# Optimization experiments

Hardware: AMD Instinct MI355X
Metric: run time of the kernel (lower is better)

Reference implementation:

```python
import jax, jax.numpy as jnp
import numpy as np

B, T, D, P = 4, 2048, 1024, 128

def setup_inputs() -> dict:
    key = jax.random.key(0)
    ks = jax.random.split(key, 10)
    inp = {
        "x": jax.random.normal(ks[0], (B, T, D), dtype=jnp.float32),
        "Q_filt": jax.random.normal(ks[1], (P, P), dtype=jnp.float32),
        "K_filt": jax.random.normal(ks[2], (P, P), dtype=jnp.float32),
        "W_in": jax.random.normal(ks[3], (D, P), dtype=jnp.float32) / np.sqrt(D),
        "b_in": jax.random.normal(ks[4], (P,), dtype=jnp.float32) * 0.01,
        "W_v": jax.random.normal(ks[5], (D, P), dtype=jnp.float32) / np.sqrt(D),
        "b_v": jax.random.normal(ks[6], (P,), dtype=jnp.float32) * 0.01,
        "W_o": jax.random.normal(ks[7], (P, D), dtype=jnp.float32) / np.sqrt(P),
        "b_o": jax.random.normal(ks[8], (D,), dtype=jnp.float32) * 0.01,
        "decay": jnp.ones((T,), dtype=jnp.float32),
    }
    return inp

def reference(x, Q_filt, K_filt, W_in, b_in, W_v, b_v, W_o, b_o, decay):
    # x: (B,T,D)
    x_proj = x @ W_in + b_in          # (B,T,P)
    Q = x_proj @ Q_filt               # (B,T,P)
    K = x_proj @ K_filt               # (B,T,P)
    V = x @ W_v + b_v                 # (B,T,P)
    # outer-product state per timestep, scaled by per-step decay
    Z = jnp.einsum('bti,btj->btij', V, K) * decay[None, :, None, None]
    H = jnp.cumsum(Z, axis=1)         # (B,T,P,P) cumulative linear-attn state
    Y = jnp.einsum('bti,btij->btj', Q, H)  # (B,T,P)
    return Y @ W_o + b_o              # (B,T,D)
```

## Files before the change

kernel.cpp:

```cpp
#include <hip/hip_runtime.h>

#define BB 4
#define TT 2048
#define DD 1024
#define PP 128
#define NC 16
#define CH 128

typedef __attribute__((ext_vector_type(8))) short bf16x8;
typedef __attribute__((ext_vector_type(4))) float f32x4;

__device__ inline ushort f2bf(float f) {
  unsigned u = __builtin_bit_cast(unsigned, f);
  u = (u + 0x7FFF + ((u >> 16) & 1)) >> 16;
  return (ushort)u;
}
__device__ inline float bf2f(ushort u) {
  unsigned v = ((unsigned)u) << 16;
  return __builtin_bit_cast(float, v);
}

__device__ inline void gll16(const void* g, void* l) {
  __builtin_amdgcn_global_load_lds(
      (const __attribute__((address_space(1))) void*)g,
      (__attribute__((address_space(3))) void*)l, 16, 0, 0);
}

__device__ inline int swzoff(int row, int kbyte) {
  return row * 256 + (kbyte ^ ((row & 7) << 4));
}
__device__ inline int swz128(int row, int kbyte) {
  return row * 128 + (kbyte ^ ((row & 7) << 4));
}

template <int NI, int NT>
__device__ inline void stage_swz(const ushort* __restrict__ g, int ld, int koff,
                                 char* lds, int tid) {
#pragma unroll
  for (int j = 0; j < NI; ++j) {
    int L = j * (NT * 16) + tid * 16;
    int row = L >> 8;
    int off = (L & 255) ^ ((row & 7) << 4);
    gll16(g + (size_t)row * ld + koff + (off >> 1),
          lds + j * (NT * 16) + ((tid & (NT - 64)) << 4));
  }
}
template <int NI, int NT>
__device__ inline void stage_swz128(const ushort* __restrict__ g, int ld,
                                    int koff, char* lds, int tid) {
#pragma unroll
  for (int j = 0; j < NI; ++j) {
    int L = j * (NT * 16) + tid * 16;
    int row = L >> 7;
    int off = (L & 127) ^ ((row & 7) << 4);
    gll16(g + (size_t)row * ld + koff + (off >> 1),
          lds + j * (NT * 16) + ((tid & (NT - 64)) << 4));
  }
}

__device__ inline bf16x8 ld_swz(const char* lds, int row, int kbyte) {
  return *(const bf16x8*)(lds + swzoff(row, kbyte));
}
__device__ inline bf16x8 ld_swz128(const char* lds, int row, int kbyte) {
  return *(const bf16x8*)(lds + swz128(row, kbyte));
}

__device__ inline bf16x8 pack8(const float4& a, const float4& b) {
  bf16x8 v;
  v[0] = (short)f2bf(a.x); v[1] = (short)f2bf(a.y);
  v[2] = (short)f2bf(a.z); v[3] = (short)f2bf(a.w);
  v[4] = (short)f2bf(b.x); v[5] = (short)f2bf(b.y);
  v[6] = (short)f2bf(b.z); v[7] = (short)f2bf(b.w);
  return v;
}

__global__ __launch_bounds__(256) void prep_t(
    const float* __restrict__ Qf, const float* __restrict__ Kf,
    const float* __restrict__ W_in, const float* __restrict__ b_in,
    const float* __restrict__ W_v, const float* __restrict__ b_v,
    const float* __restrict__ W_o, ushort* __restrict__ WcatT,
    ushort* __restrict__ QKcT, ushort* __restrict__ WoT,
    float* __restrict__ bcat) {
  const int bid = blockIdx.x;
  const int t = threadIdx.x;
  if (bid == 104) {
    bcat[t] = (t < 128) ? b_in[t] : b_v[t - 128];
    return;
  }
  const float* src;
  ushort* dst;
  int ld_src, ld_dst, nn0;
  if (bid < 64) {
    int tn = bid >> 4, tk = bid & 15;
    src = (tn < 2) ? W_in : W_v;
    nn0 = (tn & 1) * 64;
    ld_src = 128;
    src += (size_t)(tk * 64) * 128;
    dst = WcatT + (size_t)(tn * 64) * 1024 + tk * 64;
    ld_dst = 1024;
  } else if (bid < 96) {
    int j = bid - 64, tn = j >> 1, tk = j & 1;
    src = W_o;
    nn0 = tn * 64;
    ld_src = 1024;
    src += (size_t)(tk * 64) * 1024;
    dst = WoT + (size_t)(tn * 64) * 128 + tk * 64;
    ld_dst = 128;
  } else {
    int j = bid - 96, tn = j >> 1, tk = j & 1;
    src = (tn < 2) ? Qf : Kf;
    nn0 = (tn & 1) * 64;
    ld_src = 128;
    src += (size_t)(tk * 64) * 128;
    dst = QKcT + (size_t)(tn * 64) * 128 + tk * 64;
    ld_dst = 128;
  }
  __shared__ ushort Tt[64][68];
  const int kr = t >> 4, nc = (t & 15) * 4;
#pragma unroll
  for (int p = 0; p < 4; ++p) {
    float4 v = *(const float4*)&src[(size_t)(p * 16 + kr) * ld_src + nn0 + nc];
    Tt[p * 16 + kr][nc + 0] = f2bf(v.x);
    Tt[p * 16 + kr][nc + 1] = f2bf(v.y);
    Tt[p * 16 + kr][nc + 2] = f2bf(v.z);
    Tt[p * 16 + kr][nc + 3] = f2bf(v.w);
  }
  __syncthreads();
  const int nr = t >> 4, kc = (t & 15) * 4;
#pragma unroll
  for (int p = 0; p < 4; ++p) {
    ushort4 o;
    o.x = Tt[kc + 0][p * 16 + nr];
    o.y = Tt[kc + 1][p * 16 + nr];
    o.z = Tt[kc + 2][p * 16 + nr];
    o.w = Tt[kc + 3][p * 16 + nr];
    *(ushort4*)&dst[(size_t)(p * 16 + nr) * ld_dst + kc] = o;
  }
}

__global__ __launch_bounds__(512) void gemm_xw(
    const float* __restrict__ x, const ushort* __restrict__ WcatT,
    const ushort* __restrict__ QKcT, const float* __restrict__ bcat,
    const float* __restrict__ decay, ushort* __restrict__ Qb,
    ushort* __restrict__ KdT, ushort* __restrict__ V,
    ushort* __restrict__ VT) {
  __shared__ char sm[81920];
  const int bid = blockIdx.x;
  const int swz = (bid & 7) * 32 + (bid >> 3);
  const int bm = (swz >> 1) * 64;
  const int bn = (swz & 1) * 128;
  const int tid = threadIdx.x, w = tid >> 6, l = tid & 63;
  const int wr = w >> 2, wc = w & 3, lr = l & 15, lk = l >> 4;

  const int arow = tid >> 3;
  const int acol = (tid & 7) * 8;
  const float* Ax = x + (size_t)(bm + arow) * DD + acol;
  const ushort* Bg = WcatT + (size_t)bn * DD;

  float4 ra[2];
  f32x4 z = {0.f, 0.f, 0.f, 0.f};
  f32x4 acc[2][2];
#pragma unroll
  for (int m = 0; m < 2; ++m)
#pragma unroll
    for (int n = 0; n < 2; ++n) acc[m][n] = z;

#define LOADA(t)                                                 \
  {                                                              \
    const float4* p = (const float4*)(Ax + (((t) & 15) << 6));   \
    ra[0] = p[0];                                                \
    ra[1] = p[1];                                                \
  }
#define WRITEA(lds) \
  { *(bf16x8*)((lds) + swz128(arow, acol * 2)) = pack8(ra[0], ra[1]); }

  LOADA(0);
  stage_swz128<2, 512>(Bg, DD, 0, sm + 8192, tid);
  asm volatile("s_waitcnt vmcnt(2)" ::: "memory");
  WRITEA(sm);
  LOADA(1);

  int cur = 0;
  for (int t = 0; t < 16; ++t) {
    char* nxt = sm + (cur ^ 1) * 24576;
    stage_swz128<2, 512>(Bg, DD, ((t + 1) & 15) << 6, nxt + 8192, tid);
    asm volatile("s_waitcnt vmcnt(2)" ::: "memory");
    WRITEA(nxt);
    LOADA(t + 2);
    asm volatile("s_waitcnt lgkmcnt(0)" ::: "memory");
    __builtin_amdgcn_s_barrier();
    const char* cp = sm + cur * 24576;
#pragma unroll
    for (int ks = 0; ks < 2; ++ks) {
      const int kb = ks * 64 + lk * 16;
      bf16x8 af[2], bfp[2];
#pragma unroll
      for (int m = 0; m < 2; ++m)
        af[m] = ld_swz128(cp, wr * 32 + m * 16 + lr, kb);
#pragma unroll
      for (int n = 0; n < 2; ++n)
        bfp[n] = ld_swz128(cp + 8192, wc * 32 + n * 16 + lr, kb);
#pragma unroll
      for (int m = 0; m < 2; ++m)
#pragma unroll
        for (int n = 0; n < 2; ++n)
          acc[m][n] = __builtin_amdgcn_mfma_f32_16x16x32_bf16(af[m], bfp[n], acc[m][n], 0, 0, 0);
    }
    __builtin_amdgcn_s_barrier();
    cur ^= 1;
  }
  asm volatile("s_waitcnt vmcnt(0)" ::: "memory");
  __syncthreads();
#undef LOADA
#undef WRITEA

  if (bn == 0) {
#pragma unroll
    for (int m = 0; m < 2; ++m)
#pragma unroll
      for (int n = 0; n < 2; ++n) {
        const int rowl = wr * 32 + m * 16 + lk * 4;
        const int col = wc * 32 + n * 16 + lr;
        const float bv = bcat[col];
#pragma unroll
        for (int j = 0; j < 4; ++j)
          *(ushort*)(sm + swzoff(rowl + j, col * 2)) = f2bf(acc[m][n][j] + bv);
      }
    stage_swz<8, 512>(QKcT, PP, 0, sm + 16384, tid);
    __syncthreads();

    f32x4 a2[2][4];
#pragma unroll
    for (int m = 0; m < 2; ++m)
#pragma unroll
      for (int n = 0; n < 4; ++n) a2[m][n] = z;
#pragma unroll
    for (int ks = 0; ks < 4; ++ks) {
      const int kb = ks * 64 + lk * 16;
      bf16x8 af[2], bfp[4];
#pragma unroll
      for (int m = 0; m < 2; ++m)
        af[m] = ld_swz(sm, wr * 32 + m * 16 + lr, kb);
#pragma unroll
      for (int n = 0; n < 4; ++n)
        bfp[n] = ld_swz(sm + 16384, wc * 64 + n * 16 + lr, kb);
#pragma unroll
      for (int m = 0; m < 2; ++m)
#pragma unroll
        for (int n = 0; n < 4; ++n)
          a2[m][n] = __builtin_amdgcn_mfma_f32_16x16x32_bf16(af[m], bfp[n], a2[m][n], 0, 0, 0);
    }
    __syncthreads();

#pragma unroll
    for (int m = 0; m < 2; ++m)
#pragma unroll
      for (int n = 0; n < 4; ++n) {
        const int rowl = wr * 32 + m * 16 + lk * 4;
        const int col = wc * 64 + n * 16 + lr;
        if (col < 128) {
#pragma unroll
          for (int j = 0; j < 4; ++j)
            Qb[(size_t)(bm + rowl + j) * PP + col] = f2bf(a2[m][n][j]);
        } else {
          const int cc = col - 128;
#pragma unroll
          for (int j = 0; j < 4; ++j) {
            float v = a2[m][n][j] * decay[(bm + rowl + j) & (TT - 1)];
            *(ushort*)(sm + 16384 + swz128(cc, (rowl + j) * 2)) = f2bf(v);
          }
        }
      }
    __syncthreads();

    {
      const int cc = tid >> 2;
#pragma unroll
      for (int i = 0; i < 2; ++i) {
        const int ch = (tid & 3) * 2 + i;
        bf16x8 v = ld_swz128(sm + 16384, cc, ch * 16);
        *(bf16x8*)&KdT[(size_t)cc * (BB * TT) + bm + ch * 8] = v;
      }
    }
  } else {
    ushort(*VTt)[72] = (ushort(*)[72]) & sm[0];
#pragma unroll
    for (int m = 0; m < 2; ++m)
#pragma unroll
      for (int n = 0; n < 2; ++n) {
        const int tl = wr * 32 + m * 16 + lk * 4;
        const int cc = wc * 32 + n * 16 + lr;
        const float bv = bcat[128 + cc];
#pragma unroll
        for (int j = 0; j < 4; ++j) {
          ushort u = f2bf(acc[m][n][j] + bv);
          V[(size_t)(bm + tl + j) * PP + cc] = u;
          VTt[cc][tl + j] = u;
        }
      }
    __syncthreads();
    const int row = tid >> 2;
#pragma unroll
    for (int i = 0; i < 2; ++i) {
      const int ch = (tid & 3) * 2 + i;
      bf16x8 v = *(const bf16x8*)&VTt[row][ch * 8];
      *(bf16x8*)&VT[(size_t)row * (BB * TT) + bm + ch * 8] = v;
    }
  }
}

__global__ __launch_bounds__(256) void chunk_state(
    const ushort* __restrict__ KdT, const ushort* __restrict__ VT,
    ushort* __restrict__ Scb) {
  const int p = blockIdx.x;
  const int xcd = p & 7, idx = p >> 3;
  const int bc = xcd + 8 * (idx >> 2);
  const int q = idx & 3;
  const int qj = q >> 1, qi = q & 1;
  const size_t r0 = (size_t)(bc >> 4) * TT + (bc & 15) * CH;
  const int tid = threadIdx.x, w = tid >> 6, l = tid & 63;
  const int wr = w >> 1, wc = w & 1, lr = l & 15, lk = l >> 4;

  f32x4 z = {0.f, 0.f, 0.f, 0.f};
  f32x4 acc[2][2];
#pragma unroll
  for (int m = 0; m < 2; ++m)
#pragma unroll
    for (int n = 0; n < 2; ++n) acc[m][n] = z;
#pragma unroll
  for (int ks = 0; ks < 4; ++ks) {
    const int kk = ks * 32 + lk * 8;
    bf16x8 af[2], bf[2];
#pragma unroll
    for (int m = 0; m < 2; ++m)
      af[m] = *(const bf16x8*)&KdT[(size_t)(qj * 64 + wr * 32 + m * 16 + lr) * (BB * TT) + r0 + kk];
#pragma unroll
    for (int n = 0; n < 2; ++n)
      bf[n] = *(const bf16x8*)&VT[(size_t)(qi * 64 + wc * 32 + n * 16 + lr) * (BB * TT) + r0 + kk];
#pragma unroll
    for (int m = 0; m < 2; ++m)
#pragma unroll
      for (int n = 0; n < 2; ++n)
        acc[m][n] = __builtin_amdgcn_mfma_f32_16x16x32_bf16(af[m], bf[n], acc[m][n], 0, 0, 0);
  }
#pragma unroll
  for (int m = 0; m < 2; ++m)
#pragma unroll
    for (int n = 0; n < 2; ++n)
#pragma unroll
      for (int j = 0; j < 4; ++j)
        Scb[(size_t)bc * 16384 +
            (size_t)(qj * 64 + wr * 32 + m * 16 + lk * 4 + j) * 128 +
            (qi * 64 + wc * 32 + n * 16 + lr)] = f2bf(acc[m][n][j]);
}

__global__ __launch_bounds__(256) void chunk_scan(const ushort* __restrict__ Scb,
                                                  ushort* __restrict__ SxT) {
  const int b = blockIdx.y;
  const int e = blockIdx.x * 256 + threadIdx.x;
  float run = 0.f;
#pragma unroll
  for (int c = 0; c < NC; ++c) {
    const size_t idx = (size_t)(b * NC + c) * 16384 + e;
    SxT[idx] = f2bf(run);
    run += bf2f(Scb[idx]);
  }
}

__global__ __launch_bounds__(256) void attn_mfma(
    const ushort* __restrict__ Qb, const ushort* __restrict__ V,
    const ushort* __restrict__ KdT, const ushort* __restrict__ SxT,
    ushort* __restrict__ Y) {
  __shared__ char Am[64 * 256];
  const int p = blockIdx.x;
  const int xcd = p & 7, idx = p >> 3;
  const int bc = xcd + 8 * (idx >> 2);
  const int q = idx & 3;
  const int hr = q >> 1, hc = q & 1;
  const size_t r0 = (size_t)(bc >> 4) * TT + (bc & 15) * CH;
  const int tid = threadIdx.x, w = tid >> 6, l = tid & 63;
  const int wr = w >> 1, wc = w & 1, lr = l & 15, lk = l >> 4;

  f32x4 z = {0.f, 0.f, 0.f, 0.f};

  if (hr == 1 || wc == 0) {
    f32x4 a1[2][4];
#pragma unroll
    for (int m = 0; m < 2; ++m)
#pragma unroll
      for (int n = 0; n < 4; ++n) a1[m][n] = z;
#pragma unroll
    for (int ks = 0; ks < 4; ++ks) {
      const int kk = ks * 32 + lk * 8;
      bf16x8 af[2], bf[4];
#pragma unroll
      for (int m = 0; m < 2; ++m)
        af[m] = *(const bf16x8*)&Qb[(r0 + hr * 64 + wr * 32 + m * 16 + lr) * 128 + kk];
#pragma unroll
      for (int n = 0; n < 4; ++n)
        bf[n] = *(const bf16x8*)&V[(r0 + wc * 64 + n * 16 + lr) * 128 + kk];
#pragma unroll
      for (int m = 0; m < 2; ++m)
#pragma unroll
        for (int n = 0; n < 4; ++n)
          a1[m][n] = __builtin_amdgcn_mfma_f32_16x16x32_bf16(af[m], bf[n], a1[m][n], 0, 0, 0);
    }
#pragma unroll
    for (int m = 0; m < 2; ++m)
#pragma unroll
      for (int n = 0; n < 4; ++n)
#pragma unroll
        for (int j = 0; j < 4; ++j) {
          int tl = wr * 32 + m * 16 + lk * 4 + j;
          int t = hr * 64 + tl;
          int s = wc * 64 + n * 16 + lr;
          float v = (s <= t) ? a1[m][n][j] : 0.f;
          *(ushort*)(Am + swzoff(tl, s * 2)) = f2bf(v);
        }
  }
  __syncthreads();

  f32x4 a2[2][2];
#pragma unroll
  for (int m = 0; m < 2; ++m)
#pragma unroll
    for (int n = 0; n < 2; ++n) a2[m][n] = z;
  const int nks = hr ? 4 : 2;
  for (int ks = 0; ks < nks; ++ks) {
    const int kb = ks * 64 + lk * 16, kk = ks * 32 + lk * 8;
    bf16x8 af[2], bf[2];
#pragma unroll
    for (int m = 0; m < 2; ++m)
      af[m] = ld_swz(Am, wr * 32 + m * 16 + lr, kb);
#pragma unroll
    for (int n = 0; n < 2; ++n)
      bf[n] = *(const bf16x8*)&KdT[(size_t)(hc * 64 + wc * 32 + n * 16 + lr) * (BB * TT) + r0 + kk];
#pragma unroll
    for (int m = 0; m < 2; ++m)
#pragma unroll
      for (int n = 0; n < 2; ++n)
        a2[m][n] = __builtin_amdgcn_mfma_f32_16x16x32_bf16(af[m], bf[n], a2[m][n], 0, 0, 0);
  }
#pragma unroll
  for (int ks = 0; ks < 4; ++ks) {
    const int kk = ks * 32 + lk * 8;
    bf16x8 af[2], bf[2];
#pragma unroll
    for (int m = 0; m < 2; ++m)
      af[m] = *(const bf16x8*)&Qb[(r0 + hr * 64 + wr * 32 + m * 16 + lr) * 128 + kk];
#pragma unroll
    for (int n = 0; n < 2; ++n)
      bf[n] = *(const bf16x8*)&SxT[(size_t)bc * 16384 +
                                   (size_t)(hc * 64 + wc * 32 + n * 16 + lr) * 128 + kk];
#pragma unroll
    for (int m = 0; m < 2; ++m)
#pragma unroll
      for (int n = 0; n < 2; ++n)
        a2[m][n] = __builtin_amdgcn_mfma_f32_16x16x32_bf16(af[m], bf[n], a2[m][n], 0, 0, 0);
  }
#pragma unroll
  for (int m = 0; m < 2; ++m)
#pragma unroll
    for (int n = 0; n < 2; ++n)
#pragma unroll
      for (int j = 0; j < 4; ++j) {
        int t = hr * 64 + wr * 32 + m * 16 + lk * 4 + j;
        int col = hc * 64 + wc * 32 + n * 16 + lr;
        Y[(r0 + t) * 128 + col] = f2bf(a2[m][n][j]);
      }
}

__global__ __launch_bounds__(256) void gemm_out(
    const ushort* __restrict__ Y, const ushort* __restrict__ WoT,
    const float* __restrict__ b_o, float* __restrict__ out) {
  __shared__ char sm[49152];
  const int bid = blockIdx.x;
  const int swz = (bid & 7) * 128 + (bid >> 3);
  const int bm = (swz >> 3) * 64, bn = (swz & 7) * 128;
  const int tid = threadIdx.x, w = tid >> 6, l = tid & 63;
  const int wr = w >> 1, wc = w & 1, lr = l & 15, lk = l >> 4;
  stage_swz<4, 256>(Y + (size_t)bm * PP, PP, 0, sm, tid);
  stage_swz<8, 256>(WoT + (size_t)bn * PP, PP, 0, sm + 16384, tid);
  f32x4 z = {0.f, 0.f, 0.f, 0.f};
  f32x4 acc[2][4];
#pragma unroll
  for (int m = 0; m < 2; ++m)
#pragma unroll
    for (int n = 0; n < 4; ++n) acc[m][n] = z;
  __syncthreads();
#pragma unroll
  for (int ks = 0; ks < 4; ++ks) {
    const int kb = ks * 64 + lk * 16;
    bf16x8 af[2], bfp[4];
#pragma unroll
    for (int m = 0; m < 2; ++m) af[m] = ld_swz(sm, wr * 32 + m * 16 + lr, kb);
#pragma unroll
    for (int n = 0; n < 4; ++n)
      bfp[n] = ld_swz(sm + 16384, wc * 64 + n * 16 + lr, kb);
#pragma unroll
    for (int m = 0; m < 2; ++m)
#pragma unroll
      for (int n = 0; n < 4; ++n)
        acc[m][n] = __builtin_amdgcn_mfma_f32_16x16x32_bf16(af[m], bfp[n], acc[m][n], 0, 0, 0);
  }
#pragma unroll
  for (int m = 0; m < 2; ++m)
#pragma unroll
    for (int n = 0; n < 4; ++n) {
      const int rowb = bm + wr * 32 + m * 16 + lk * 4;
      const int col = bn + wc * 64 + n * 16 + lr;
      const float bv = b_o[col];
#pragma unroll
      for (int j = 0; j < 4; ++j)
        out[(size_t)(rowb + j) * DD + col] = acc[m][n][j] + bv;
    }
}

extern "C" void kernel_launch(void* const* d_in, const int* in_sizes, int n_in,
                              void* d_out, int out_size, void* d_ws, size_t ws_size,
                              hipStream_t stream) {
  const float* x = (const float*)d_in[0];
  const float* Qf = (const float*)d_in[1];
  const float* Kf = (const float*)d_in[2];
  const float* W_in = (const float*)d_in[3];
  const float* b_in = (const float*)d_in[4];
  const float* W_v = (const float*)d_in[5];
  const float* b_v = (const float*)d_in[6];
  const float* W_o = (const float*)d_in[7];
  const float* b_o = (const float*)d_in[8];
  const float* decay = (const float*)d_in[9];
  float* out = (float*)d_out;
  char* W = (char*)d_ws;

  ushort* V     = (ushort*)(W);
  ushort* VT    = (ushort*)(W + 2097152);
  ushort* Qb    = (ushort*)(W + 4194304);
  ushort* KdT   = (ushort*)(W + 6291456);
  ushort* Scb   = (ushort*)(W + 8388608);
  ushort* SxT   = (ushort*)(W + 10485760);
  ushort* Yb    = (ushort*)(W + 12582912);
  ushort* WcatT = (ushort*)(W + 14680064);
  ushort* QKcT  = (ushort*)(W + 15204352);
  ushort* WoT   = (ushort*)(W + 15269888);
  float*  bcat  = (float*)(W + 15532032);

  prep_t<<<105, 256, 0, stream>>>(Qf, Kf, W_in, b_in, W_v, b_v, W_o,
                                  WcatT, QKcT, WoT, bcat);
  gemm_xw<<<256, 512, 0, stream>>>(x, WcatT, QKcT, bcat, decay,
                                   Qb, KdT, V, VT);
  chunk_state<<<256, 256, 0, stream>>>(KdT, VT, Scb);
  chunk_scan<<<dim3(64, BB), 256, 0, stream>>>(Scb, SxT);
  attn_mfma<<<256, 256, 0, stream>>>(Qb, V, KdT, SxT, Yb);
  gemm_out<<<1024, 256, 0, stream>>>(Yb, WoT, b_o, out);
}
```

Baseline: 47.89 us.

## Fuse chunk state, scan and attention into one persistent kernel with grid barriers

```diff
diff --git a/kernel.cpp b/kernel.cpp
--- a/kernel.cpp
+++ b/kernel.cpp
@@ -72,6 +72,19 @@
   v[4] = (short)f2bf(b.x); v[5] = (short)f2bf(b.y);
   v[6] = (short)f2bf(b.z); v[7] = (short)f2bf(b.w);
   return v;
+}
+
+__device__ inline void grid_bar(unsigned* flags, int p, unsigned target, int tid) {
+  __syncthreads();
+  if (tid == 0) {
+    __threadfence();
+    __hip_atomic_store(&flags[p], target, __ATOMIC_RELEASE,
+                       __HIP_MEMORY_SCOPE_AGENT);
+  }
+  while (__hip_atomic_load(&flags[tid], __ATOMIC_ACQUIRE,
+                           __HIP_MEMORY_SCOPE_AGENT) < target)
+    __builtin_amdgcn_s_sleep(1);
+  __syncthreads();
 }
 
 __global__ __launch_bounds__(256) void prep_t(
@@ -309,165 +322,162 @@
   }
 }
 
-__global__ __launch_bounds__(256) void chunk_state(
+__global__ __launch_bounds__(256) void state_attn(
+    const ushort* __restrict__ Qb, const ushort* __restrict__ V,
     const ushort* __restrict__ KdT, const ushort* __restrict__ VT,
-    ushort* __restrict__ Scb) {
+    ushort* __restrict__ Scb, ushort* __restrict__ SxT,
+    ushort* __restrict__ Y, unsigned* __restrict__ flags) {
+  __shared__ char Am[64 * 256];
   const int p = blockIdx.x;
-  const int xcd = p & 7, idx = p >> 3;
-  const int bc = xcd + 8 * (idx >> 2);
-  const int q = idx & 3;
-  const int qj = q >> 1, qi = q & 1;
-  const size_t r0 = (size_t)(bc >> 4) * TT + (bc & 15) * CH;
   const int tid = threadIdx.x, w = tid >> 6, l = tid & 63;
   const int wr = w >> 1, wc = w & 1, lr = l & 15, lk = l >> 4;
-
   f32x4 z = {0.f, 0.f, 0.f, 0.f};
-  f32x4 acc[2][2];
-#pragma unroll
-  for (int m = 0; m < 2; ++m)
-#pragma unroll
-    for (int n = 0; n < 2; ++n) acc[m][n] = z;
-#pragma unroll
-  for (int ks = 0; ks < 4; ++ks) {
-    const int kk = ks * 32 + lk * 8;
-    bf16x8 af[2], bf[2];
-#pragma unroll
-    for (int m = 0; m < 2; ++m)
-      af[m] = *(const bf16x8*)&KdT[(size_t)(qj * 64 + wr * 32 + m * 16 + lr) * (BB * TT) + r0 + kk];
-#pragma unroll
-    for (int n = 0; n < 2; ++n)
-      bf[n] = *(const bf16x8*)&VT[(size_t)(qi * 64 + wc * 32 + n * 16 + lr) * (BB * TT) + r0 + kk];
-#pragma unroll
-    for (int m = 0; m < 2; ++m)
-#pragma unroll
-      for (int n = 0; n < 2; ++n)
-        acc[m][n] = __builtin_amdgcn_mfma_f32_16x16x32_bf16(af[m], bf[n], acc[m][n], 0, 0, 0);
-  }
-#pragma unroll
-  for (int m = 0; m < 2; ++m)
-#pragma unroll
-    for (int n = 0; n < 2; ++n)
-#pragma unroll
-      for (int j = 0; j < 4; ++j)
-        Scb[(size_t)bc * 16384 +
-            (size_t)(qj * 64 + wr * 32 + m * 16 + lk * 4 + j) * 128 +
-            (qi * 64 + wc * 32 + n * 16 + lr)] = f2bf(acc[m][n][j]);
-}
-
-__global__ __launch_bounds__(256) void chunk_scan(const ushort* __restrict__ Scb,
-                                                  ushort* __restrict__ SxT) {
-  const int b = blockIdx.y;
-  const int e = blockIdx.x * 256 + threadIdx.x;
-  float run = 0.f;
-#pragma unroll
-  for (int c = 0; c < NC; ++c) {
-    const size_t idx = (size_t)(b * NC + c) * 16384 + e;
-    SxT[idx] = f2bf(run);
-    run += bf2f(Scb[idx]);
-  }
-}
-
-__global__ __launch_bounds__(256) void attn_mfma(
-    const ushort* __restrict__ Qb, const ushort* __restrict__ V,
-    const ushort* __restrict__ KdT, const ushort* __restrict__ SxT,
-    ushort* __restrict__ Y) {
-  __shared__ char Am[64 * 256];
-  const int p = blockIdx.x;
-  const int xcd = p & 7, idx = p >> 3;
-  const int bc = xcd + 8 * (idx >> 2);
-  const int q = idx & 3;
-  const int hr = q >> 1, hc = q & 1;
-  const size_t r0 = (size_t)(bc >> 4) * TT + (bc & 15) * CH;
-  const int tid = threadIdx.x, w = tid >> 6, l = tid & 63;
-  const int wr = w >> 1, wc = w & 1, lr = l & 15, lk = l >> 4;
-
-  f32x4 z = {0.f, 0.f, 0.f, 0.f};
-
-  if (hr == 1 || wc == 0) {
-    f32x4 a1[2][4];
-#pragma unroll
-    for (int m = 0; m < 2; ++m)
-#pragma unroll
-      for (int n = 0; n < 4; ++n) a1[m][n] = z;
+
+  {
+    const int xcd = p & 7, idx = p >> 3;
+    const int bc = xcd + 8 * (idx >> 2);
+    const int q = idx & 3;
+    const int qj = q >> 1, qi = q & 1;
+    const size_t r0 = (size_t)(bc >> 4) * TT + (bc & 15) * CH;
+    f32x4 acc[2][2];
+#pragma unroll
+    for (int m = 0; m < 2; ++m)
+#pragma unroll
+      for (int n = 0; n < 2; ++n) acc[m][n] = z;
 #pragma unroll
     for (int ks = 0; ks < 4; ++ks) {
       const int kk = ks * 32 + lk * 8;
-      bf16x8 af[2], bf[4];
+      bf16x8 af[2], bf[2];
+#pragma unroll
+      for (int m = 0; m < 2; ++m)
+        af[m] = *(const bf16x8*)&KdT[(size_t)(qj * 64 + wr * 32 + m * 16 + lr) * (BB * TT) + r0 + kk];
+#pragma unroll
+      for (int n = 0; n < 2; ++n)
+        bf[n] = *(const bf16x8*)&VT[(size_t)(qi * 64 + wc * 32 + n * 16 + lr) * (BB * TT) + r0 + kk];
+#pragma unroll
+      for (int m = 0; m < 2; ++m)
+#pragma unroll
+        for (int n = 0; n < 2; ++n)
+          acc[m][n] = __builtin_amdgcn_mfma_f32_16x16x32_bf16(af[m], bf[n], acc[m][n], 0, 0, 0);
+    }
+#pragma unroll
+    for (int m = 0; m < 2; ++m)
+#pragma unroll
+      for (int n = 0; n < 2; ++n)
+#pragma unroll
+        for (int j = 0; j < 4; ++j)
+          Scb[(size_t)bc * 16384 +
+              (size_t)(qj * 64 + wr * 32 + m * 16 + lk * 4 + j) * 128 +
+              (qi * 64 + wc * 32 + n * 16 + lr)] = f2bf(acc[m][n][j]);
+  }
+  grid_bar(flags, p, 1u, tid);
+
+  {
+    const int b = p >> 6;
+    const int e = (p & 63) * 256 + tid;
+    float run = 0.f;
+#pragma unroll
+    for (int c = 0; c < NC; ++c) {
+      const size_t idx = (size_t)(b * NC + c) * 16384 + e;
+      SxT[idx] = f2bf(run);
+      run += bf2f(Scb[idx]);
+    }
+  }
+  grid_bar(flags, p, 2u, tid);
+
+  {
+    const int xcd = p & 7, idx = p >> 3;
+    const int bc = xcd + 8 * (idx >> 2);
+    const int q = idx & 3;
+    const int hr = q >> 1, hc = q & 1;
+    const size_t r0 = (size_t)(bc >> 4) * TT + (bc & 15) * CH;
+
+    if (hr == 1 || wc == 0) {
+      f32x4 a1[2][4];
+#pragma unroll
+      for (int m = 0; m < 2; ++m)
+#pragma unroll
+        for (int n = 0; n < 4; ++n) a1[m][n] = z;
+#pragma unroll
+      for (int ks = 0; ks < 4; ++ks) {
+        const int kk = ks * 32 + lk * 8;
+        bf16x8 af[2], bf[4];
+#pragma unroll
+        for (int m = 0; m < 2; ++m)
+          af[m] = *(const bf16x8*)&Qb[(r0 + hr * 64 + wr * 32 + m * 16 + lr) * 128 + kk];
+#pragma unroll
+        for (int n = 0; n < 4; ++n)
+          bf[n] = *(const bf16x8*)&V[(r0 + wc * 64 + n * 16 + lr) * 128 + kk];
+#pragma unroll
+        for (int m = 0; m < 2; ++m)
+#pragma unroll
+          for (int n = 0; n < 4; ++n)
+            a1[m][n] = __builtin_amdgcn_mfma_f32_16x16x32_bf16(af[m], bf[n], a1[m][n], 0, 0, 0);
+      }
+#pragma unroll
+      for (int m = 0; m < 2; ++m)
+#pragma unroll
+        for (int n = 0; n < 4; ++n)
+#pragma unroll
+          for (int j = 0; j < 4; ++j) {
+            int tl = wr * 32 + m * 16 + lk * 4 + j;
+            int t = hr * 64 + tl;
+            int s = wc * 64 + n * 16 + lr;
+            float v = (s <= t) ? a1[m][n][j] : 0.f;
+            *(ushort*)(Am + swzoff(tl, s * 2)) = f2bf(v);
+          }
+    }
+    __syncthreads();
+
+    f32x4 a2[2][2];
+#pragma unroll
+    for (int m = 0; m < 2; ++m)
+#pragma unroll
+      for (int n = 0; n < 2; ++n) a2[m][n] = z;
+    const int nks = hr ? 4 : 2;
+    for (int ks = 0; ks < nks; ++ks) {
+      const int kb = ks * 64 + lk * 16, kk = ks * 32 + lk * 8;
+      bf16x8 af[2], bf[2];
+#pragma unroll
+      for (int m = 0; m < 2; ++m)
+        af[m] = ld_swz(Am, wr * 32 + m * 16 + lr, kb);
+#pragma unroll
+      for (int n = 0; n < 2; ++n)
+        bf[n] = *(const bf16x8*)&KdT[(size_t)(hc * 64 + wc * 32 + n * 16 + lr) * (BB * TT) + r0 + kk];
+#pragma unroll
+      for (int m = 0; m < 2; ++m)
+#pragma unroll
+        for (int n = 0; n < 2; ++n)
+          a2[m][n] = __builtin_amdgcn_mfma_f32_16x16x32_bf16(af[m], bf[n], a2[m][n], 0, 0, 0);
+    }
+#pragma unroll
+    for (int ks = 0; ks < 4; ++ks) {
+      const int kk = ks * 32 + lk * 8;
+      bf16x8 af[2], bf[2];
 #pragma unroll
       for (int m = 0; m < 2; ++m)
         af[m] = *(const bf16x8*)&Qb[(r0 + hr * 64 + wr * 32 + m * 16 + lr) * 128 + kk];
 #pragma unroll
-      for (int n = 0; n < 4; ++n)
-        bf[n] = *(const bf16x8*)&V[(r0 + wc * 64 + n * 16 + lr) * 128 + kk];
-#pragma unroll
-      for (int m = 0; m < 2; ++m)
-#pragma unroll
-        for (int n = 0; n < 4; ++n)
-          a1[m][n] = __builtin_amdgcn_mfma_f32_16x16x32_bf16(af[m], bf[n], a1[m][n], 0, 0, 0);
-    }
-#pragma unroll
-    for (int m = 0; m < 2; ++m)
-#pragma unroll
-      for (int n = 0; n < 4; ++n)
+      for (int n = 0; n < 2; ++n)
+        bf[n] = *(const bf16x8*)&SxT[(size_t)bc * 16384 +
+                                     (size_t)(hc * 64 + wc * 32 + n * 16 + lr) * 128 + kk];
+#pragma unroll
+      for (int m = 0; m < 2; ++m)
+#pragma unroll
+        for (int n = 0; n < 2; ++n)
+          a2[m][n] = __builtin_amdgcn_mfma_f32_16x16x32_bf16(af[m], bf[n], a2[m][n], 0, 0, 0);
+    }
+#pragma unroll
+    for (int m = 0; m < 2; ++m)
+#pragma unroll
+      for (int n = 0; n < 2; ++n)
 #pragma unroll
         for (int j = 0; j < 4; ++j) {
-          int tl = wr * 32 + m * 16 + lk * 4 + j;
-          int t = hr * 64 + tl;
-          int s = wc * 64 + n * 16 + lr;
-          float v = (s <= t) ? a1[m][n][j] : 0.f;
-          *(ushort*)(Am + swzoff(tl, s * 2)) = f2bf(v);
+          int t = hr * 64 + wr * 32 + m * 16 + lk * 4 + j;
+          int col = hc * 64 + wc * 32 + n * 16 + lr;
+          Y[(r0 + t) * 128 + col] = f2bf(a2[m][n][j]);
         }
   }
-  __syncthreads();
-
-  f32x4 a2[2][2];
-#pragma unroll
-  for (int m = 0; m < 2; ++m)
-#pragma unroll
-    for (int n = 0; n < 2; ++n) a2[m][n] = z;
-  const int nks = hr ? 4 : 2;
-  for (int ks = 0; ks < nks; ++ks) {
-    const int kb = ks * 64 + lk * 16, kk = ks * 32 + lk * 8;
-    bf16x8 af[2], bf[2];
-#pragma unroll
-    for (int m = 0; m < 2; ++m)
-      af[m] = ld_swz(Am, wr * 32 + m * 16 + lr, kb);
-#pragma unroll
-    for (int n = 0; n < 2; ++n)
-      bf[n] = *(const bf16x8*)&KdT[(size_t)(hc * 64 + wc * 32 + n * 16 + lr) * (BB * TT) + r0 + kk];
-#pragma unroll
-    for (int m = 0; m < 2; ++m)
-#pragma unroll
-      for (int n = 0; n < 2; ++n)
-        a2[m][n] = __builtin_amdgcn_mfma_f32_16x16x32_bf16(af[m], bf[n], a2[m][n], 0, 0, 0);
-  }
-#pragma unroll
-  for (int ks = 0; ks < 4; ++ks) {
-    const int kk = ks * 32 + lk * 8;
-    bf16x8 af[2], bf[2];
-#pragma unroll
-    for (int m = 0; m < 2; ++m)
-      af[m] = *(const bf16x8*)&Qb[(r0 + hr * 64 + wr * 32 + m * 16 + lr) * 128 + kk];
-#pragma unroll
-    for (int n = 0; n < 2; ++n)
-      bf[n] = *(const bf16x8*)&SxT[(size_t)bc * 16384 +
-                                   (size_t)(hc * 64 + wc * 32 + n * 16 + lr) * 128 + kk];
-#pragma unroll
-    for (int m = 0; m < 2; ++m)
-#pragma unroll
-      for (int n = 0; n < 2; ++n)
-        a2[m][n] = __builtin_amdgcn_mfma_f32_16x16x32_bf16(af[m], bf[n], a2[m][n], 0, 0, 0);
-  }
-#pragma unroll
-  for (int m = 0; m < 2; ++m)
-#pragma unroll
-    for (int n = 0; n < 2; ++n)
-#pragma unroll
-      for (int j = 0; j < 4; ++j) {
-        int t = hr * 64 + wr * 32 + m * 16 + lk * 4 + j;
-        int col = hc * 64 + wc * 32 + n * 16 + lr;
-        Y[(r0 + t) * 128 + col] = f2bf(a2[m][n][j]);
-      }
 }
 
 __global__ __launch_bounds__(256) void gemm_out(
@@ -543,13 +553,13 @@
   ushort* QKcT  = (ushort*)(W + 15204352);
   ushort* WoT   = (ushort*)(W + 15269888);
   float*  bcat  = (float*)(W + 15532032);
-
+  unsigned* flags = (unsigned*)(W + 15536128);
+
+  hipMemsetAsync(flags, 0, 256 * sizeof(unsigned), stream);
   prep_t<<<105, 256, 0, stream>>>(Qf, Kf, W_in, b_in, W_v, b_v, W_o,
                                   WcatT, QKcT, WoT, bcat);
   gemm_xw<<<256, 512, 0, stream>>>(x, WcatT, QKcT, bcat, decay,
                                    Qb, KdT, V, VT);
-  chunk_state<<<256, 256, 0, stream>>>(KdT, VT, Scb);
-  chunk_scan<<<dim3(64, BB), 256, 0, stream>>>(Scb, SxT);
-  attn_mfma<<<256, 256, 0, stream>>>(Qb, V, KdT, SxT, Yb);
+  state_attn<<<256, 256, 0, stream>>>(Qb, V, KdT, VT, Scb, SxT, Yb, flags);
   gemm_out<<<1024, 256, 0, stream>>>(Yb, WoT, b_o, out);
 }
```

After: 117.7 us. +145.7%, slower.
